# Kernel tuning notes

Measured on AMD Instinct MI355X. Metric: run time of the kernel, lower is better.

## Reference

```python
import jax, jax.numpy as jnp
import numpy as np

N, NFEAT, NHID, NCLASS = 2048, 128, 32, 16

def setup_inputs() -> dict:
    key = jax.random.key(0)
    ks = jax.random.split(key, 12)
    scale = 1.0 / np.sqrt(N)
    inp = {
        "x_init": jax.random.normal(ks[0], (N, NFEAT), jnp.float32),
        "adj": jax.random.uniform(ks[1], (N, N), jnp.float32),
        "adj1_org": jax.random.normal(ks[2], (N, N), jnp.float32) * scale,
        "fully_connected_graph": jnp.ones((N, N), jnp.int32),
        # gc1: GraphConvolution(nfeat, nhid)
        "W1": jax.random.normal(ks[3], (NFEAT, NHID), jnp.float32) / np.sqrt(NFEAT),
        "b1": jnp.zeros((NHID,), jnp.float32),
        # gc2: GraphConvolution(nhid + nfeat, nclass)
        "W2": jax.random.normal(ks[4], (NHID + NFEAT, NCLASS), jnp.float32) / np.sqrt(NHID + NFEAT),
        "b2": jnp.zeros((NCLASS,), jnp.float32),
        # confidence: Linear(2*nhid, nhid) -> Linear(nhid, 1)
        "Wc1": jax.random.normal(ks[5], (2 * NHID, NHID), jnp.float32) / np.sqrt(2 * NHID),
        "bc1": jnp.zeros((NHID,), jnp.float32),
        "Wc2": jax.random.normal(ks[6], (NHID, 1), jnp.float32) / np.sqrt(NHID),
        "bc2": jnp.zeros((1,), jnp.float32),
    }
    return inp

def reference(x_init, adj, adj1_org, fully_connected_graph,
              W1, b1, W2, b2, Wc1, bc1, Wc2, bc2):
    # gc1: adj1_org @ (x_init @ W1) + b1, then tanh (dropout is identity in eval)
    x = jnp.tanh(adj1_org @ (x_init @ W1) + b1)  # [N, nhid]
    # confidence MLP over pairwise concat([x_i, x_j]):
    # Linear(cat([xi,xj])) == xi@Wa + xj@Wb + bc1, with Wc1 = [Wa; Wb]
    Wa, Wb = jnp.split(Wc1, 2, axis=0)
    hidden = (x @ Wa + bc1)[:, None, :] + (x @ Wb)[None, :, :]  # [N, N, nhid]
    e = hidden @ Wc2[:, 0] + bc2[0]  # [N, N] edge score
    # masked_fill(e > 0, 1) then squeeze
    scores = jnp.where(e > 0, 1.0, e)
    adj1 = adj1_org * scores
    xc = jnp.concatenate([x, x_init], axis=-1)  # [N, nhid + nfeat]
    out = adj1 @ (xc @ W2) + b2  # [N, nclass]
    return jax.nn.log_softmax(out, axis=1)
```

## Files before the change

kernel.cpp:

```cpp
#include <hip/hip_runtime.h>
#include <hip/hip_bf16.h>
#include <math.h>

#define N 2048
#define NFEAT 128
#define NHID 32
#define NCLASS 16
#define NSTRIP 16
#define KS 128

#define WS_T1    0
#define WS_Y0    65536
#define WS_WA    98304
#define WS_WB    98336
#define WS_CB    98368
#define WS_PART2 98432
#define WS_Y     1147008
#define WS_PC    1179776
#define WS_Q     1181824
#define WS_PART3 1183872

__global__ __launch_bounds__(256) void k1_prep(
    const float* __restrict__ x_init, const float* __restrict__ W1,
    const float* __restrict__ W2, const float* __restrict__ Wc1,
    const float* __restrict__ bc1, const float* __restrict__ Wc2,
    const float* __restrict__ bc2, float* __restrict__ ws)
{
    __shared__ float xs[8 * 128];
    __shared__ float W1s[128 * 32];
    __shared__ float W2bs[128 * 16];
    int t = threadIdx.x;
    int blk = blockIdx.x;

    *reinterpret_cast<float4*>(&xs[4 * t]) =
        *reinterpret_cast<const float4*>(&x_init[blk * 1024 + 4 * t]);
    #pragma unroll
    for (int i = 0; i < 4; ++i) {
        int f = t + 256 * i;
        *reinterpret_cast<float4*>(&W1s[4 * f]) =
            *reinterpret_cast<const float4*>(&W1[4 * f]);
    }
    #pragma unroll
    for (int i = 0; i < 2; ++i) {
        int f = t + 256 * i;
        *reinterpret_cast<float4*>(&W2bs[4 * f]) =
            *reinterpret_cast<const float4*>(&W2[512 + 4 * f]);
    }
    __syncthreads();

    int rl = t >> 5, c = t & 31;
    int r = blk * 8 + rl;

    float acc = 0.f;
    #pragma unroll 8
    for (int k = 0; k < 128; ++k) acc = fmaf(xs[rl * 128 + k], W1s[k * 32 + c], acc);
    ws[WS_T1 + r * 32 + c] = acc;

    if (c < 16) {
        float a2 = 0.f;
        #pragma unroll 8
        for (int k = 0; k < 128; ++k) a2 = fmaf(xs[rl * 128 + k], W2bs[k * 16 + c], a2);
        ws[WS_Y0 + r * 16 + c] = a2;
    }

    if (blk == 0 && t < 32) {
        float wa = 0.f, wb = 0.f;
        for (int h = 0; h < 32; ++h) {
            float w = Wc2[h];
            wa = fmaf(Wc1[t * 32 + h], w, wa);
            wb = fmaf(Wc1[(32 + t) * 32 + h], w, wb);
        }
        ws[WS_WA + t] = wa;
        ws[WS_WB + t] = wb;
        if (t == 0) {
            float cb = bc2[0];
            for (int h = 0; h < 32; ++h) cb = fmaf(bc1[h], Wc2[h], cb);
            ws[WS_CB] = cb;
        }
    }
}

__global__ __launch_bounds__(256, 2) void k2_mm(
    const float* __restrict__ A, const float* __restrict__ ws_in,
    float* __restrict__ ws_out)
{
    __shared__ float As[64][132];
    __shared__ float Bs[128][32];

    const float* t1 = ws_in + WS_T1;
    int t = threadIdx.x;
    int rt = blockIdx.x >> 4;
    int ks = blockIdx.x & 15;
    int row0 = rt * 64;
    int jbase = ks * KS;

    #pragma unroll
    for (int i = 0; i < 8; ++i) {
        int f = t + 256 * i;
        int r = f >> 5, c4 = f & 31;
        float4 v = *reinterpret_cast<const float4*>(
            &A[(size_t)(row0 + r) * N + jbase + 4 * c4]);
        *reinterpret_cast<float4*>(&As[r][4 * c4]) = v;
    }
    #pragma unroll
    for (int i = 0; i < 4; ++i) {
        int f = t + 256 * i;
        int r = f >> 3, c4 = f & 7;
        float4 v = *reinterpret_cast<const float4*>(&t1[(jbase + r) * 32 + 4 * c4]);
        *reinterpret_cast<float4*>(&Bs[r][4 * c4]) = v;
    }
    __syncthreads();

    int cg = t & 7;
    int rg = t >> 3;

    float acc0[4] = {0.f, 0.f, 0.f, 0.f};
    float acc1[4] = {0.f, 0.f, 0.f, 0.f};

    #pragma unroll
    for (int kq = 0; kq < 32; ++kq) {
        float4 a0 = *reinterpret_cast<const float4*>(&As[rg][4 * kq]);
        float4 a1 = *reinterpret_cast<const float4*>(&As[rg + 32][4 * kq]);
        float4 b0 = *reinterpret_cast<const float4*>(&Bs[4 * kq + 0][4 * cg]);
        float4 b1 = *reinterpret_cast<const float4*>(&Bs[4 * kq + 1][4 * cg]);
        float4 b2 = *reinterpret_cast<const float4*>(&Bs[4 * kq + 2][4 * cg]);
        float4 b3 = *reinterpret_cast<const float4*>(&Bs[4 * kq + 3][4 * cg]);

        acc0[0] = fmaf(a0.x, b0.x, acc0[0]); acc0[1] = fmaf(a0.x, b0.y, acc0[1]);
        acc0[2] = fmaf(a0.x, b0.z, acc0[2]); acc0[3] = fmaf(a0.x, b0.w, acc0[3]);
        acc1[0] = fmaf(a1.x, b0.x, acc1[0]); acc1[1] = fmaf(a1.x, b0.y, acc1[1]);
        acc1[2] = fmaf(a1.x, b0.z, acc1[2]); acc1[3] = fmaf(a1.x, b0.w, acc1[3]);

        acc0[0] = fmaf(a0.y, b1.x, acc0[0]); acc0[1] = fmaf(a0.y, b1.y, acc0[1]);
        acc0[2] = fmaf(a0.y, b1.z, acc0[2]); acc0[3] = fmaf(a0.y, b1.w, acc0[3]);
        acc1[0] = fmaf(a1.y, b1.x, acc1[0]); acc1[1] = fmaf(a1.y, b1.y, acc1[1]);
        acc1[2] = fmaf(a1.y, b1.z, acc1[2]); acc1[3] = fmaf(a1.y, b1.w, acc1[3]);

        acc0[0] = fmaf(a0.z, b2.x, acc0[0]); acc0[1] = fmaf(a0.z, b2.y, acc0[1]);
        acc0[2] = fmaf(a0.z, b2.z, acc0[2]); acc0[3] = fmaf(a0.z, b2.w, acc0[3]);
        acc1[0] = fmaf(a1.z, b2.x, acc1[0]); acc1[1] = fmaf(a1.z, b2.y, acc1[1]);
        acc1[2] = fmaf(a1.z, b2.z, acc1[2]); acc1[3] = fmaf(a1.z, b2.w, acc1[3]);

        acc0[0] = fmaf(a0.w, b3.x, acc0[0]); acc0[1] = fmaf(a0.w, b3.y, acc0[1]);
        acc0[2] = fmaf(a0.w, b3.z, acc0[2]); acc0[3] = fmaf(a0.w, b3.w, acc0[3]);
        acc1[0] = fmaf(a1.w, b3.x, acc1[0]); acc1[1] = fmaf(a1.w, b3.y, acc1[1]);
        acc1[2] = fmaf(a1.w, b3.z, acc1[2]); acc1[3] = fmaf(a1.w, b3.w, acc1[3]);
    }

    float* o0 = ws_out + WS_PART2 + ((size_t)(ks * N + row0 + rg)) * 32 + 4 * cg;
    float* o1 = ws_out + WS_PART2 + ((size_t)(ks * N + row0 + rg + 32)) * 32 + 4 * cg;
    *reinterpret_cast<float4*>(o0) = make_float4(acc0[0], acc0[1], acc0[2], acc0[3]);
    *reinterpret_cast<float4*>(o1) = make_float4(acc1[0], acc1[1], acc1[2], acc1[3]);
}

__global__ __launch_bounds__(256) void k2b_post(
    const float* __restrict__ b1, const float* __restrict__ W2,
    float* __restrict__ ws)
{
    __shared__ float xs[8][32];
    int t = threadIdx.x;
    int rl = t >> 5, c = t & 31;
    int r = blockIdx.x * 8 + rl;

    const float* p2 = ws + WS_PART2;
    float s = b1[c];
    #pragma unroll
    for (int ks = 0; ks < NSTRIP; ++ks)
        s += p2[(size_t)(ks * N + r) * 32 + c];
    float x = tanhf(s);
    xs[rl][c] = x;
    __syncthreads();

    float pp = x * ws[WS_WA + c];
    float qq = x * ws[WS_WB + c];
    #pragma unroll
    for (int d = 1; d < 32; d <<= 1) {
        pp += __shfl_xor(pp, d);
        qq += __shfl_xor(qq, d);
    }
    if (c == 0) {
        ws[WS_PC + r] = pp + ws[WS_CB];
        ws[WS_Q + r] = qq;
    }

    if (c < 16) {
        float acc = ws[WS_Y0 + r * 16 + c];
        #pragma unroll 8
        for (int h = 0; h < 32; ++h) acc = fmaf(xs[rl][h], W2[h * 16 + c], acc);
        ws[WS_Y + r * 16 + c] = acc;
    }
}

__global__ __launch_bounds__(256, 2) void k3_mm(
    const float* __restrict__ A, const float* __restrict__ ws_in,
    float* __restrict__ ws_out)
{
    __shared__ float As[64][132];
    __shared__ float Bs[128][16];

    const float* y = ws_in + WS_Y;
    const float* qv = ws_in + WS_Q;
    const float* pc = ws_in + WS_PC;
    int t = threadIdx.x;
    int rt = blockIdx.x >> 4;
    int ks = blockIdx.x & 15;
    int row0 = rt * 64;
    int jbase = ks * KS;

    #pragma unroll
    for (int i = 0; i < 8; ++i) {
        int f = t + 256 * i;
        int r = f >> 5, c4 = f & 31;
        int j0 = jbase + 4 * c4;
        float4 a = *reinterpret_cast<const float4*>(&A[(size_t)(row0 + r) * N + j0]);
        float4 q4 = *reinterpret_cast<const float4*>(&qv[j0]);
        float pcr = pc[row0 + r];
        float e0 = pcr + q4.x, e1 = pcr + q4.y, e2 = pcr + q4.z, e3 = pcr + q4.w;
        float4 cf;
        cf.x = a.x * ((e0 > 0.f) ? 1.f : e0);
        cf.y = a.y * ((e1 > 0.f) ? 1.f : e1);
        cf.z = a.z * ((e2 > 0.f) ? 1.f : e2);
        cf.w = a.w * ((e3 > 0.f) ? 1.f : e3);
        *reinterpret_cast<float4*>(&As[r][4 * c4]) = cf;
    }
    #pragma unroll
    for (int i = 0; i < 2; ++i) {
        int f = t + 256 * i;
        int r = f >> 2, c4 = f & 3;
        float4 v = *reinterpret_cast<const float4*>(&y[(jbase + r) * 16 + 4 * c4]);
        *reinterpret_cast<float4*>(&Bs[r][4 * c4]) = v;
    }
    __syncthreads();

    int cg = t & 3;
    int rg = t >> 2;

    float acc[4] = {0.f, 0.f, 0.f, 0.f};

    #pragma unroll
    for (int kq = 0; kq < 32; ++kq) {
        float4 a = *reinterpret_cast<const float4*>(&As[rg][4 * kq]);
        float4 b0 = *reinterpret_cast<const float4*>(&Bs[4 * kq + 0][4 * cg]);
        float4 b1 = *reinterpret_cast<const float4*>(&Bs[4 * kq + 1][4 * cg]);
        float4 b2 = *reinterpret_cast<const float4*>(&Bs[4 * kq + 2][4 * cg]);
        float4 b3 = *reinterpret_cast<const float4*>(&Bs[4 * kq + 3][4 * cg]);

        acc[0] = fmaf(a.x, b0.x, acc[0]); acc[1] = fmaf(a.x, b0.y, acc[1]);
        acc[2] = fmaf(a.x, b0.z, acc[2]); acc[3] = fmaf(a.x, b0.w, acc[3]);
        acc[0] = fmaf(a.y, b1.x, acc[0]); acc[1] = fmaf(a.y, b1.y, acc[1]);
        acc[2] = fmaf(a.y, b1.z, acc[2]); acc[3] = fmaf(a.y, b1.w, acc[3]);
        acc[0] = fmaf(a.z, b2.x, acc[0]); acc[1] = fmaf(a.z, b2.y, acc[1]);
        acc[2] = fmaf(a.z, b2.z, acc[2]); acc[3] = fmaf(a.z, b2.w, acc[3]);
        acc[0] = fmaf(a.w, b3.x, acc[0]); acc[1] = fmaf(a.w, b3.y, acc[1]);
        acc[2] = fmaf(a.w, b3.z, acc[2]); acc[3] = fmaf(a.w, b3.w, acc[3]);
    }

    float* o = ws_out + WS_PART3 + ((size_t)(ks * N + row0 + rg)) * 16 + 4 * cg;
    *reinterpret_cast<float4*>(o) = make_float4(acc[0], acc[1], acc[2], acc[3]);
}

__global__ __launch_bounds__(256) void k3b_lsm(
    const float* __restrict__ b2, const float* __restrict__ ws,
    float* __restrict__ out)
{
    int t = threadIdx.x;
    int rl = t >> 4, c = t & 15;
    int r = blockIdx.x * 16 + rl;

    const float* p3 = ws + WS_PART3;
    float o = b2[c];
    #pragma unroll
    for (int ks = 0; ks < NSTRIP; ++ks)
        o += p3[(size_t)(ks * N + r) * 16 + c];

    float m = o;
    #pragma unroll
    for (int d = 1; d < 16; d <<= 1) m = fmaxf(m, __shfl_xor(m, d));
    float ex = expf(o - m);
    float sm = ex;
    #pragma unroll
    for (int d = 1; d < 16; d <<= 1) sm += __shfl_xor(sm, d);

    out[r * 16 + c] = o - m - logf(sm);
}

extern "C" void kernel_launch(void* const* d_in, const int* in_sizes, int n_in,
                              void* d_out, int out_size, void* d_ws, size_t ws_size,
                              hipStream_t stream)
{
    const float* x_init = (const float*)d_in[0];
    const float* adj1   = (const float*)d_in[2];
    const float* W1  = (const float*)d_in[4];
    const float* b1  = (const float*)d_in[5];
    const float* W2  = (const float*)d_in[6];
    const float* b2  = (const float*)d_in[7];
    const float* Wc1 = (const float*)d_in[8];
    const float* bc1 = (const float*)d_in[9];
    const float* Wc2 = (const float*)d_in[10];
    const float* bc2 = (const float*)d_in[11];
    float* out = (float*)d_out;
    float* ws = (float*)d_ws;

    hipLaunchKernelGGL(k1_prep, dim3(256), dim3(256), 0, stream,
                       x_init, W1, W2, Wc1, bc1, Wc2, bc2, ws);
    hipLaunchKernelGGL(k2_mm, dim3(512), dim3(256), 0, stream, adj1, ws, ws);
    hipLaunchKernelGGL(k2b_post, dim3(256), dim3(256), 0, stream, b1, W2, ws);
    hipLaunchKernelGGL(k3_mm, dim3(512), dim3(256), 0, stream, adj1, ws, ws);
    hipLaunchKernelGGL(k3b_lsm, dim3(128), dim3(256), 0, stream, b2, ws, out);
}
```

Measured before the change: 123.0 us.

## Retile split-K matmuls to 128x64 tiles with 32 strips and XOR-swizzled LDS

Both adjacency matmul kernels now use 128-row by 64-column tiles with 32 K-strips instead of 64x128 with 16 strips. Each thread computes more rows, and the A tile in shared memory is stored with an XOR swizzle in place of padding to avoid bank conflicts. The intent is more reuse of B per A load and fewer LDS conflicts. In exchange, the partial-sum buffers double in size and the reduction kernels must sum twice as many strips.

```diff
diff --git a/kernel.cpp b/kernel.cpp
--- a/kernel.cpp
+++ b/kernel.cpp
@@ -6,8 +6,8 @@
 #define NFEAT 128
 #define NHID 32
 #define NCLASS 16
-#define NSTRIP 16
-#define KS 128
+#define NSTRIP 32
+#define KS 64
 
 #define WS_T1    0
 #define WS_Y0    65536
@@ -15,10 +15,10 @@
 #define WS_WB    98336
 #define WS_CB    98368
 #define WS_PART2 98432
-#define WS_Y     1147008
-#define WS_PC    1179776
-#define WS_Q     1181824
-#define WS_PART3 1183872
+#define WS_Y     2195584
+#define WS_PC    2228352
+#define WS_Q     2230400
+#define WS_PART3 2232448
 
 __global__ __launch_bounds__(256) void k1_prep(
     const float* __restrict__ x_init, const float* __restrict__ W1,
@@ -84,73 +84,100 @@
     const float* __restrict__ A, const float* __restrict__ ws_in,
     float* __restrict__ ws_out)
 {
-    __shared__ float As[64][132];
-    __shared__ float Bs[128][32];
+    __shared__ float As[128 * 64];
+    __shared__ float Bs[64 * 32];
 
     const float* t1 = ws_in + WS_T1;
     int t = threadIdx.x;
-    int rt = blockIdx.x >> 4;
-    int ks = blockIdx.x & 15;
-    int row0 = rt * 64;
+    int rt = blockIdx.x >> 5;
+    int ks = blockIdx.x & 31;
+    int row0 = rt * 128;
     int jbase = ks * KS;
 
     #pragma unroll
     for (int i = 0; i < 8; ++i) {
         int f = t + 256 * i;
-        int r = f >> 5, c4 = f & 31;
+        int r = f >> 4, u = f & 15;
         float4 v = *reinterpret_cast<const float4*>(
-            &A[(size_t)(row0 + r) * N + jbase + 4 * c4]);
-        *reinterpret_cast<float4*>(&As[r][4 * c4]) = v;
-    }
-    #pragma unroll
-    for (int i = 0; i < 4; ++i) {
+            &A[(size_t)(row0 + r) * N + jbase + 4 * u]);
+        *reinterpret_cast<float4*>(&As[4 * (r * 16 + (u ^ (r & 7)))]) = v;
+    }
+    #pragma unroll
+    for (int i = 0; i < 2; ++i) {
         int f = t + 256 * i;
         int r = f >> 3, c4 = f & 7;
         float4 v = *reinterpret_cast<const float4*>(&t1[(jbase + r) * 32 + 4 * c4]);
-        *reinterpret_cast<float4*>(&Bs[r][4 * c4]) = v;
+        *reinterpret_cast<float4*>(&Bs[r * 32 + 4 * c4]) = v;
     }
     __syncthreads();
 
+    int rg = t >> 3;
     int cg = t & 7;
-    int rg = t >> 3;
+    int rsw = rg & 7;
 
     float acc0[4] = {0.f, 0.f, 0.f, 0.f};
     float acc1[4] = {0.f, 0.f, 0.f, 0.f};
-
-    #pragma unroll
-    for (int kq = 0; kq < 32; ++kq) {
-        float4 a0 = *reinterpret_cast<const float4*>(&As[rg][4 * kq]);
-        float4 a1 = *reinterpret_cast<const float4*>(&As[rg + 32][4 * kq]);
-        float4 b0 = *reinterpret_cast<const float4*>(&Bs[4 * kq + 0][4 * cg]);
-        float4 b1 = *reinterpret_cast<const float4*>(&Bs[4 * kq + 1][4 * cg]);
-        float4 b2 = *reinterpret_cast<const float4*>(&Bs[4 * kq + 2][4 * cg]);
-        float4 b3 = *reinterpret_cast<const float4*>(&Bs[4 * kq + 3][4 * cg]);
+    float acc2[4] = {0.f, 0.f, 0.f, 0.f};
+    float acc3[4] = {0.f, 0.f, 0.f, 0.f};
+
+    #pragma unroll
+    for (int kq = 0; kq < 16; ++kq) {
+        int ku = kq ^ rsw;
+        float4 a0 = *reinterpret_cast<const float4*>(&As[4 * ((rg +  0) * 16 + ku)]);
+        float4 a1 = *reinterpret_cast<const float4*>(&As[4 * ((rg + 32) * 16 + ku)]);
+        float4 a2 = *reinterpret_cast<const float4*>(&As[4 * ((rg + 64) * 16 + ku)]);
+        float4 a3 = *reinterpret_cast<const float4*>(&As[4 * ((rg + 96) * 16 + ku)]);
+        float4 b0 = *reinterpret_cast<const float4*>(&Bs[(4 * kq + 0) * 32 + 4 * cg]);
+        float4 b1 = *reinterpret_cast<const float4*>(&Bs[(4 * kq + 1) * 32 + 4 * cg]);
+        float4 b2 = *reinterpret_cast<const float4*>(&Bs[(4 * kq + 2) * 32 + 4 * cg]);
+        float4 b3 = *reinterpret_cast<const float4*>(&Bs[(4 * kq + 3) * 32 + 4 * cg]);
 
         acc0[0] = fmaf(a0.x, b0.x, acc0[0]); acc0[1] = fmaf(a0.x, b0.y, acc0[1]);
         acc0[2] = fmaf(a0.x, b0.z, acc0[2]); acc0[3] = fmaf(a0.x, b0.w, acc0[3]);
+        acc0[0] = fmaf(a0.y, b1.x, acc0[0]); acc0[1] = fmaf(a0.y, b1.y, acc0[1]);
+        acc0[2] = fmaf(a0.y, b1.z, acc0[2]); acc0[3] = fmaf(a0.y, b1.w, acc0[3]);
+        acc0[0] = fmaf(a0.z, b2.x, acc0[0]); acc0[1] = fmaf(a0.z, b2.y, acc0[1]);
+        acc0[2] = fmaf(a0.z, b2.z, acc0[2]); acc0[3] = fmaf(a0.z, b2.w, acc0[3]);
+        acc0[0] = fmaf(a0.w, b3.x, acc0[0]); acc0[1] = fmaf(a0.w, b3.y, acc0[1]);
+        acc0[2] = fmaf(a0.w, b3.z, acc0[2]); acc0[3] = fmaf(a0.w, b3.w, acc0[3]);
+
         acc1[0] = fmaf(a1.x, b0.x, acc1[0]); acc1[1] = fmaf(a1.x, b0.y, acc1[1]);
         acc1[2] = fmaf(a1.x, b0.z, acc1[2]); acc1[3] = fmaf(a1.x, b0.w, acc1[3]);
-
-        acc0[0] = fmaf(a0.y, b1.x, acc0[0]); acc0[1] = fmaf(a0.y, b1.y, acc0[1]);
-        acc0[2] = fmaf(a0.y, b1.z, acc0[2]); acc0[3] = fmaf(a0.y, b1.w, acc0[3]);
         acc1[0] = fmaf(a1.y, b1.x, acc1[0]); acc1[1] = fmaf(a1.y, b1.y, acc1[1]);
         acc1[2] = fmaf(a1.y, b1.z, acc1[2]); acc1[3] = fmaf(a1.y, b1.w, acc1[3]);
-
-        acc0[0] = fmaf(a0.z, b2.x, acc0[0]); acc0[1] = fmaf(a0.z, b2.y, acc0[1]);
-        acc0[2] = fmaf(a0.z, b2.z, acc0[2]); acc0[3] = fmaf(a0.z, b2.w, acc0[3]);
         acc1[0] = fmaf(a1.z, b2.x, acc1[0]); acc1[1] = fmaf(a1.z, b2.y, acc1[1]);
         acc1[2] = fmaf(a1.z, b2.z, acc1[2]); acc1[3] = fmaf(a1.z, b2.w, acc1[3]);
-
-        acc0[0] = fmaf(a0.w, b3.x, acc0[0]); acc0[1] = fmaf(a0.w, b3.y, acc0[1]);
-        acc0[2] = fmaf(a0.w, b3.z, acc0[2]); acc0[3] = fmaf(a0.w, b3.w, acc0[3]);
         acc1[0] = fmaf(a1.w, b3.x, acc1[0]); acc1[1] = fmaf(a1.w, b3.y, acc1[1]);
         acc1[2] = fmaf(a1.w, b3.z, acc1[2]); acc1[3] = fmaf(a1.w, b3.w, acc1[3]);
-    }
-
-    float* o0 = ws_out + WS_PART2 + ((size_t)(ks * N + row0 + rg)) * 32 + 4 * cg;
-    float* o1 = ws_out + WS_PART2 + ((size_t)(ks * N + row0 + rg + 32)) * 32 + 4 * cg;
-    *reinterpret_cast<float4*>(o0) = make_float4(acc0[0], acc0[1], acc0[2], acc0[3]);
-    *reinterpret_cast<float4*>(o1) = make_float4(acc1[0], acc1[1], acc1[2], acc1[3]);
+
+        acc2[0] = fmaf(a2.x, b0.x, acc2[0]); acc2[1] = fmaf(a2.x, b0.y, acc2[1]);
+        acc2[2] = fmaf(a2.x, b0.z, acc2[2]); acc2[3] = fmaf(a2.x, b0.w, acc2[3]);
+        acc2[0] = fmaf(a2.y, b1.x, acc2[0]); acc2[1] = fmaf(a2.y, b1.y, acc2[1]);
+        acc2[2] = fmaf(a2.y, b1.z, acc2[2]); acc2[3] = fmaf(a2.y, b1.w, acc2[3]);
+        acc2[0] = fmaf(a2.z, b2.x, acc2[0]); acc2[1] = fmaf(a2.z, b2.y, acc2[1]);
+        acc2[2] = fmaf(a2.z, b2.z, acc2[2]); acc2[3] = fmaf(a2.z, b2.w, acc2[3]);
+        acc2[0] = fmaf(a2.w, b3.x, acc2[0]); acc2[1] = fmaf(a2.w, b3.y, acc2[1]);
+        acc2[2] = fmaf(a2.w, b3.z, acc2[2]); acc2[3] = fmaf(a2.w, b3.w, acc2[3]);
+
+        acc3[0] = fmaf(a3.x, b0.x, acc3[0]); acc3[1] = fmaf(a3.x, b0.y, acc3[1]);
+        acc3[2] = fmaf(a3.x, b0.z, acc3[2]); acc3[3] = fmaf(a3.x, b0.w, acc3[3]);
+        acc3[0] = fmaf(a3.y, b1.x, acc3[0]); acc3[1] = fmaf(a3.y, b1.y, acc3[1]);
+        acc3[2] = fmaf(a3.y, b1.z, acc3[2]); acc3[3] = fmaf(a3.y, b1.w, acc3[3]);
+        acc3[0] = fmaf(a3.z, b2.x, acc3[0]); acc3[1] = fmaf(a3.z, b2.y, acc3[1]);
+        acc3[2] = fmaf(a3.z, b2.z, acc3[2]); acc3[3] = fmaf(a3.z, b2.w, acc3[3]);
+        acc3[0] = fmaf(a3.w, b3.x, acc3[0]); acc3[1] = fmaf(a3.w, b3.y, acc3[1]);
+        acc3[2] = fmaf(a3.w, b3.z, acc3[2]); acc3[3] = fmaf(a3.w, b3.w, acc3[3]);
+    }
+
+    float* base = ws_out + WS_PART2 + ((size_t)ks * N) * 32 + 4 * cg;
+    *reinterpret_cast<float4*>(base + (size_t)(row0 + rg +  0) * 32) =
+        make_float4(acc0[0], acc0[1], acc0[2], acc0[3]);
+    *reinterpret_cast<float4*>(base + (size_t)(row0 + rg + 32) * 32) =
+        make_float4(acc1[0], acc1[1], acc1[2], acc1[3]);
+    *reinterpret_cast<float4*>(base + (size_t)(row0 + rg + 64) * 32) =
+        make_float4(acc2[0], acc2[1], acc2[2], acc2[3]);
+    *reinterpret_cast<float4*>(base + (size_t)(row0 + rg + 96) * 32) =
+        make_float4(acc3[0], acc3[1], acc3[2], acc3[3]);
 }
 
 __global__ __launch_bounds__(256) void k2b_post(
@@ -195,23 +222,23 @@
     const float* __restrict__ A, const float* __restrict__ ws_in,
     float* __restrict__ ws_out)
 {
-    __shared__ float As[64][132];
-    __shared__ float Bs[128][16];
+    __shared__ float As[128 * 64];
+    __shared__ float Bs[64 * 16];
 
     const float* y = ws_in + WS_Y;
     const float* qv = ws_in + WS_Q;
     const float* pc = ws_in + WS_PC;
     int t = threadIdx.x;
-    int rt = blockIdx.x >> 4;
-    int ks = blockIdx.x & 15;
-    int row0 = rt * 64;
+    int rt = blockIdx.x >> 5;
+    int ks = blockIdx.x & 31;
+    int row0 = rt * 128;
     int jbase = ks * KS;
 
     #pragma unroll
     for (int i = 0; i < 8; ++i) {
         int f = t + 256 * i;
-        int r = f >> 5, c4 = f & 31;
-        int j0 = jbase + 4 * c4;
+        int r = f >> 4, u = f & 15;
+        int j0 = jbase + 4 * u;
         float4 a = *reinterpret_cast<const float4*>(&A[(size_t)(row0 + r) * N + j0]);
         float4 q4 = *reinterpret_cast<const float4*>(&qv[j0]);
         float pcr = pc[row0 + r];
@@ -221,42 +248,56 @@
         cf.y = a.y * ((e1 > 0.f) ? 1.f : e1);
         cf.z = a.z * ((e2 > 0.f) ? 1.f : e2);
         cf.w = a.w * ((e3 > 0.f) ? 1.f : e3);
-        *reinterpret_cast<float4*>(&As[r][4 * c4]) = cf;
-    }
-    #pragma unroll
-    for (int i = 0; i < 2; ++i) {
-        int f = t + 256 * i;
-        int r = f >> 2, c4 = f & 3;
+        *reinterpret_cast<float4*>(&As[4 * (r * 16 + (u ^ (r & 7)))]) = cf;
+    }
+    {
+        int r = t >> 2, c4 = t & 3;
         float4 v = *reinterpret_cast<const float4*>(&y[(jbase + r) * 16 + 4 * c4]);
-        *reinterpret_cast<float4*>(&Bs[r][4 * c4]) = v;
+        *reinterpret_cast<float4*>(&Bs[r * 16 + 4 * c4]) = v;
     }
     __syncthreads();
 
+    int rg = t >> 2;
     int cg = t & 3;
-    int rg = t >> 2;
-
-    float acc[4] = {0.f, 0.f, 0.f, 0.f};
-
-    #pragma unroll
-    for (int kq = 0; kq < 32; ++kq) {
-        float4 a = *reinterpret_cast<const float4*>(&As[rg][4 * kq]);
-        float4 b0 = *reinterpret_cast<const float4*>(&Bs[4 * kq + 0][4 * cg]);
-        float4 b1 = *reinterpret_cast<const float4*>(&Bs[4 * kq + 1][4 * cg]);
-        float4 b2 = *reinterpret_cast<const float4*>(&Bs[4 * kq + 2][4 * cg]);
-        float4 b3 = *reinterpret_cast<const float4*>(&Bs[4 * kq + 3][4 * cg]);
-
-        acc[0] = fmaf(a.x, b0.x, acc[0]); acc[1] = fmaf(a.x, b0.y, acc[1]);
-        acc[2] = fmaf(a.x, b0.z, acc[2]); acc[3] = fmaf(a.x, b0.w, acc[3]);
-        acc[0] = fmaf(a.y, b1.x, acc[0]); acc[1] = fmaf(a.y, b1.y, acc[1]);
-        acc[2] = fmaf(a.y, b1.z, acc[2]); acc[3] = fmaf(a.y, b1.w, acc[3]);
-        acc[0] = fmaf(a.z, b2.x, acc[0]); acc[1] = fmaf(a.z, b2.y, acc[1]);
-        acc[2] = fmaf(a.z, b2.z, acc[2]); acc[3] = fmaf(a.z, b2.w, acc[3]);
-        acc[0] = fmaf(a.w, b3.x, acc[0]); acc[1] = fmaf(a.w, b3.y, acc[1]);
-        acc[2] = fmaf(a.w, b3.z, acc[2]); acc[3] = fmaf(a.w, b3.w, acc[3]);
-    }
-
-    float* o = ws_out + WS_PART3 + ((size_t)(ks * N + row0 + rg)) * 16 + 4 * cg;
-    *reinterpret_cast<float4*>(o) = make_float4(acc[0], acc[1], acc[2], acc[3]);
+    int rsw = rg & 7;
+
+    float acc0[4] = {0.f, 0.f, 0.f, 0.f};
+    float acc1[4] = {0.f, 0.f, 0.f, 0.f};
+
+    #pragma unroll
+    for (int kq = 0; kq < 16; ++kq) {
+        int ku = kq ^ rsw;
+        float4 a0 = *reinterpret_cast<const float4*>(&As[4 * ((rg +  0) * 16 + ku)]);
+        float4 a1 = *reinterpret_cast<const float4*>(&As[4 * ((rg + 64) * 16 + ku)]);
+        float4 b0 = *reinterpret_cast<const float4*>(&Bs[(4 * kq + 0) * 16 + 4 * cg]);
+        float4 b1 = *reinterpret_cast<const float4*>(&Bs[(4 * kq + 1) * 16 + 4 * cg]);
+        float4 b2 = *reinterpret_cast<const float4*>(&Bs[(4 * kq + 2) * 16 + 4 * cg]);
+        float4 b3 = *reinterpret_cast<const float4*>(&Bs[(4 * kq + 3) * 16 + 4 * cg]);
+
+        acc0[0] = fmaf(a0.x, b0.x, acc0[0]); acc0[1] = fmaf(a0.x, b0.y, acc0[1]);
+        acc0[2] = fmaf(a0.x, b0.z, acc0[2]); acc0[3] = fmaf(a0.x, b0.w, acc0[3]);
+        acc0[0] = fmaf(a0.y, b1.x, acc0[0]); acc0[1] = fmaf(a0.y, b1.y, acc0[1]);
+        acc0[2] = fmaf(a0.y, b1.z, acc0[2]); acc0[3] = fmaf(a0.y, b1.w, acc0[3]);
+        acc0[0] = fmaf(a0.z, b2.x, acc0[0]); acc0[1] = fmaf(a0.z, b2.y, acc0[1]);
+        acc0[2] = fmaf(a0.z, b2.z, acc0[2]); acc0[3] = fmaf(a0.z, b2.w, acc0[3]);
+        acc0[0] = fmaf(a0.w, b3.x, acc0[0]); acc0[1] = fmaf(a0.w, b3.y, acc0[1]);
+        acc0[2] = fmaf(a0.w, b3.z, acc0[2]); acc0[3] = fmaf(a0.w, b3.w, acc0[3]);
+
+        acc1[0] = fmaf(a1.x, b0.x, acc1[0]); acc1[1] = fmaf(a1.x, b0.y, acc1[1]);
+        acc1[2] = fmaf(a1.x, b0.z, acc1[2]); acc1[3] = fmaf(a1.x, b0.w, acc1[3]);
+        acc1[0] = fmaf(a1.y, b1.x, acc1[0]); acc1[1] = fmaf(a1.y, b1.y, acc1[1]);
+        acc1[2] = fmaf(a1.y, b1.z, acc1[2]); acc1[3] = fmaf(a1.y, b1.w, acc1[3]);
+        acc1[0] = fmaf(a1.z, b2.x, acc1[0]); acc1[1] = fmaf(a1.z, b2.y, acc1[1]);
+        acc1[2] = fmaf(a1.z, b2.z, acc1[2]); acc1[3] = fmaf(a1.z, b2.w, acc1[3]);
+        acc1[0] = fmaf(a1.w, b3.x, acc1[0]); acc1[1] = fmaf(a1.w, b3.y, acc1[1]);
+        acc1[2] = fmaf(a1.w, b3.z, acc1[2]); acc1[3] = fmaf(a1.w, b3.w, acc1[3]);
+    }
+
+    float* base = ws_out + WS_PART3 + ((size_t)ks * N) * 16 + 4 * cg;
+    *reinterpret_cast<float4*>(base + (size_t)(row0 + rg +  0) * 16) =
+        make_float4(acc0[0], acc0[1], acc0[2], acc0[3]);
+    *reinterpret_cast<float4*>(base + (size_t)(row0 + rg + 64) * 16) =
+        make_float4(acc1[0], acc1[1], acc1[2], acc1[3]);
 }
 
 __global__ __launch_bounds__(256) void k3b_lsm(
```

New measurement: 124.0 us. No clear change (+0.8%).

## Fuse split-K reductions into matmul kernels via last-block atomic counters

Applied to the files above, without the earlier changes.

Removes the separate k2b_post and k3b_lsm kernels. The last block to finish each row tile, detected with a per-tile atomic counter and threadfences, now does the partial-sum reduction, tanh, projections and log-softmax for that tile. This cuts two kernel launches and their launch gaps. The cost is a serialized tail, since only 32 blocks do the reduction work, plus atomic and fence overhead. Counters are reset in k1_prep, with 32 threads zeroing 32 entries.

```diff
diff --git a/kernel.cpp b/kernel.cpp
--- a/kernel.cpp
+++ b/kernel.cpp
@@ -19,6 +19,8 @@
 #define WS_PC    1179776
 #define WS_Q     1181824
 #define WS_PART3 1183872
+#define WS_CTR2  1708160
+#define WS_CTR3  1708192
 
 __global__ __launch_bounds__(256) void k1_prep(
     const float* __restrict__ x_init, const float* __restrict__ W1,
@@ -72,6 +74,8 @@
         }
         ws[WS_WA + t] = wa;
         ws[WS_WB + t] = wb;
+        reinterpret_cast<int*>(ws + WS_CTR2)[t] = 0;
+        reinterpret_cast<int*>(ws + WS_CTR3)[t] = 0;
         if (t == 0) {
             float cb = bc2[0];
             for (int h = 0; h < 32; ++h) cb = fmaf(bc1[h], Wc2[h], cb);
@@ -81,13 +85,13 @@
 }
 
 __global__ __launch_bounds__(256, 2) void k2_mm(
-    const float* __restrict__ A, const float* __restrict__ ws_in,
-    float* __restrict__ ws_out)
+    const float* __restrict__ A, const float* __restrict__ b1,
+    const float* __restrict__ W2, float* __restrict__ ws)
 {
     __shared__ float As[64][132];
     __shared__ float Bs[128][32];
 
-    const float* t1 = ws_in + WS_T1;
+    const float* t1 = ws + WS_T1;
     int t = threadIdx.x;
     int rt = blockIdx.x >> 4;
     int ks = blockIdx.x & 15;
@@ -122,85 +126,95 @@
         float4 a0 = *reinterpret_cast<const float4*>(&As[rg][4 * kq]);
         float4 a1 = *reinterpret_cast<const float4*>(&As[rg + 32][4 * kq]);
         float4 b0 = *reinterpret_cast<const float4*>(&Bs[4 * kq + 0][4 * cg]);
-        float4 b1 = *reinterpret_cast<const float4*>(&Bs[4 * kq + 1][4 * cg]);
-        float4 b2 = *reinterpret_cast<const float4*>(&Bs[4 * kq + 2][4 * cg]);
-        float4 b3 = *reinterpret_cast<const float4*>(&Bs[4 * kq + 3][4 * cg]);
+        float4 b1v = *reinterpret_cast<const float4*>(&Bs[4 * kq + 1][4 * cg]);
+        float4 b2v = *reinterpret_cast<const float4*>(&Bs[4 * kq + 2][4 * cg]);
+        float4 b3v = *reinterpret_cast<const float4*>(&Bs[4 * kq + 3][4 * cg]);
 
         acc0[0] = fmaf(a0.x, b0.x, acc0[0]); acc0[1] = fmaf(a0.x, b0.y, acc0[1]);
         acc0[2] = fmaf(a0.x, b0.z, acc0[2]); acc0[3] = fmaf(a0.x, b0.w, acc0[3]);
         acc1[0] = fmaf(a1.x, b0.x, acc1[0]); acc1[1] = fmaf(a1.x, b0.y, acc1[1]);
         acc1[2] = fmaf(a1.x, b0.z, acc1[2]); acc1[3] = fmaf(a1.x, b0.w, acc1[3]);
 
-        acc0[0] = fmaf(a0.y, b1.x, acc0[0]); acc0[1] = fmaf(a0.y, b1.y, acc0[1]);
-        acc0[2] = fmaf(a0.y, b1.z, acc0[2]); acc0[3] = fmaf(a0.y, b1.w, acc0[3]);
-        acc1[0] = fmaf(a1.y, b1.x, acc1[0]); acc1[1] = fmaf(a1.y, b1.y, acc1[1]);
-        acc1[2] = fmaf(a1.y, b1.z, acc1[2]); acc1[3] = fmaf(a1.y, b1.w, acc1[3]);
-
-        acc0[0] = fmaf(a0.z, b2.x, acc0[0]); acc0[1] = fmaf(a0.z, b2.y, acc0[1]);
-        acc0[2] = fmaf(a0.z, b2.z, acc0[2]); acc0[3] = fmaf(a0.z, b2.w, acc0[3]);
-        acc1[0] = fmaf(a1.z, b2.x, acc1[0]); acc1[1] = fmaf(a1.z, b2.y, acc1[1]);
-        acc1[2] = fmaf(a1.z, b2.z, acc1[2]); acc1[3] = fmaf(a1.z, b2.w, acc1[3]);
-
-        acc0[0] = fmaf(a0.w, b3.x, acc0[0]); acc0[1] = fmaf(a0.w, b3.y, acc0[1]);
-        acc0[2] = fmaf(a0.w, b3.z, acc0[2]); acc0[3] = fmaf(a0.w, b3.w, acc0[3]);
-        acc1[0] = fmaf(a1.w, b3.x, acc1[0]); acc1[1] = fmaf(a1.w, b3.y, acc1[1]);
-        acc1[2] = fmaf(a1.w, b3.z, acc1[2]); acc1[3] = fmaf(a1.w, b3.w, acc1[3]);
-    }
-
-    float* o0 = ws_out + WS_PART2 + ((size_t)(ks * N + row0 + rg)) * 32 + 4 * cg;
-    float* o1 = ws_out + WS_PART2 + ((size_t)(ks * N + row0 + rg + 32)) * 32 + 4 * cg;
+        acc0[0] = fmaf(a0.y, b1v.x, acc0[0]); acc0[1] = fmaf(a0.y, b1v.y, acc0[1]);
+        acc0[2] = fmaf(a0.y, b1v.z, acc0[2]); acc0[3] = fmaf(a0.y, b1v.w, acc0[3]);
+        acc1[0] = fmaf(a1.y, b1v.x, acc1[0]); acc1[1] = fmaf(a1.y, b1v.y, acc1[1]);
+        acc1[2] = fmaf(a1.y, b1v.z, acc1[2]); acc1[3] = fmaf(a1.y, b1v.w, acc1[3]);
+
+        acc0[0] = fmaf(a0.z, b2v.x, acc0[0]); acc0[1] = fmaf(a0.z, b2v.y, acc0[1]);
+        acc0[2] = fmaf(a0.z, b2v.z, acc0[2]); acc0[3] = fmaf(a0.z, b2v.w, acc0[3]);
+        acc1[0] = fmaf(a1.z, b2v.x, acc1[0]); acc1[1] = fmaf(a1.z, b2v.y, acc1[1]);
+        acc1[2] = fmaf(a1.z, b2v.z, acc1[2]); acc1[3] = fmaf(a1.z, b2v.w, acc1[3]);
+
+        acc0[0] = fmaf(a0.w, b3v.x, acc0[0]); acc0[1] = fmaf(a0.w, b3v.y, acc0[1]);
+        acc0[2] = fmaf(a0.w, b3v.z, acc0[2]); acc0[3] = fmaf(a0.w, b3v.w, acc0[3]);
+        acc1[0] = fmaf(a1.w, b3v.x, acc1[0]); acc1[1] = fmaf(a1.w, b3v.y, acc1[1]);
+        acc1[2] = fmaf(a1.w, b3v.z, acc1[2]); acc1[3] = fmaf(a1.w, b3v.w, acc1[3]);
+    }
+
+    float* o0 = ws + WS_PART2 + ((size_t)(ks * N + row0 + rg)) * 32 + 4 * cg;
+    float* o1 = ws + WS_PART2 + ((size_t)(ks * N + row0 + rg + 32)) * 32 + 4 * cg;
     *reinterpret_cast<float4*>(o0) = make_float4(acc0[0], acc0[1], acc0[2], acc0[3]);
     *reinterpret_cast<float4*>(o1) = make_float4(acc1[0], acc1[1], acc1[2], acc1[3]);
+
+    __threadfence();
+    __syncthreads();
+    __shared__ int lastFlag;
+    if (t == 0) {
+        int* ctr = reinterpret_cast<int*>(ws + WS_CTR2);
+        lastFlag = (atomicAdd(&ctr[rt], 1) == NSTRIP - 1);
+    }
+    __syncthreads();
+    if (!lastFlag) return;
+    __threadfence();
+
+    __shared__ float xr[8][33];
+    const float* p2 = ws + WS_PART2;
+    int rl = t >> 5, c = t & 31;
+    float wa = ws[WS_WA + c];
+    float wb = ws[WS_WB + c];
+    float cb = ws[WS_CB];
+
+    for (int it = 0; it < 8; ++it) {
+        int r = row0 + it * 8 + rl;
+        float s = b1[c];
+        #pragma unroll
+        for (int k2s = 0; k2s < NSTRIP; ++k2s)
+            s += p2[(size_t)(k2s * N + r) * 32 + c];
+        float x = tanhf(s);
+        xr[rl][c] = x;
+        __syncthreads();
+
+        float pp = x * wa;
+        float qq = x * wb;
+        #pragma unroll
+        for (int d = 1; d < 32; d <<= 1) {
+            pp += __shfl_xor(pp, d);
+            qq += __shfl_xor(qq, d);
+        }
+        if (c == 0) {
+            ws[WS_PC + r] = pp + cb;
+            ws[WS_Q + r] = qq;
+        }
+        if (c < 16) {
+            float acc = ws[WS_Y0 + r * 16 + c];
+            #pragma unroll 8
+            for (int h = 0; h < 32; ++h) acc = fmaf(xr[rl][h], W2[h * 16 + c], acc);
+            ws[WS_Y + r * 16 + c] = acc;
+        }
+        __syncthreads();
+    }
 }
 
-__global__ __launch_bounds__(256) void k2b_post(
-    const float* __restrict__ b1, const float* __restrict__ W2,
-    float* __restrict__ ws)
-{
-    __shared__ float xs[8][32];
-    int t = threadIdx.x;
-    int rl = t >> 5, c = t & 31;
-    int r = blockIdx.x * 8 + rl;
-
-    const float* p2 = ws + WS_PART2;
-    float s = b1[c];
-    #pragma unroll
-    for (int ks = 0; ks < NSTRIP; ++ks)
-        s += p2[(size_t)(ks * N + r) * 32 + c];
-    float x = tanhf(s);
-    xs[rl][c] = x;
-    __syncthreads();
-
-    float pp = x * ws[WS_WA + c];
-    float qq = x * ws[WS_WB + c];
-    #pragma unroll
-    for (int d = 1; d < 32; d <<= 1) {
-        pp += __shfl_xor(pp, d);
-        qq += __shfl_xor(qq, d);
-    }
-    if (c == 0) {
-        ws[WS_PC + r] = pp + ws[WS_CB];
-        ws[WS_Q + r] = qq;
-    }
-
-    if (c < 16) {
-        float acc = ws[WS_Y0 + r * 16 + c];
-        #pragma unroll 8
-        for (int h = 0; h < 32; ++h) acc = fmaf(xs[rl][h], W2[h * 16 + c], acc);
-        ws[WS_Y + r * 16 + c] = acc;
-    }
-}
-
 __global__ __launch_bounds__(256, 2) void k3_mm(
-    const float* __restrict__ A, const float* __restrict__ ws_in,
-    float* __restrict__ ws_out)
+    const float* __restrict__ A, const float* __restrict__ b2,
+    float* __restrict__ ws, float* __restrict__ out)
 {
     __shared__ float As[64][132];
     __shared__ float Bs[128][16];
 
-    const float* y = ws_in + WS_Y;
-    const float* qv = ws_in + WS_Q;
-    const float* pc = ws_in + WS_PC;
+    const float* y = ws + WS_Y;
+    const float* qv = ws + WS_Q;
+    const float* pc = ws + WS_PC;
     int t = threadIdx.x;
     int rt = blockIdx.x >> 4;
     int ks = blockIdx.x & 15;
@@ -241,47 +255,54 @@
     for (int kq = 0; kq < 32; ++kq) {
         float4 a = *reinterpret_cast<const float4*>(&As[rg][4 * kq]);
         float4 b0 = *reinterpret_cast<const float4*>(&Bs[4 * kq + 0][4 * cg]);
-        float4 b1 = *reinterpret_cast<const float4*>(&Bs[4 * kq + 1][4 * cg]);
-        float4 b2 = *reinterpret_cast<const float4*>(&Bs[4 * kq + 2][4 * cg]);
-        float4 b3 = *reinterpret_cast<const float4*>(&Bs[4 * kq + 3][4 * cg]);
+        float4 b1v = *reinterpret_cast<const float4*>(&Bs[4 * kq + 1][4 * cg]);
+        float4 b2v = *reinterpret_cast<const float4*>(&Bs[4 * kq + 2][4 * cg]);
+        float4 b3v = *reinterpret_cast<const float4*>(&Bs[4 * kq + 3][4 * cg]);
 
         acc[0] = fmaf(a.x, b0.x, acc[0]); acc[1] = fmaf(a.x, b0.y, acc[1]);
         acc[2] = fmaf(a.x, b0.z, acc[2]); acc[3] = fmaf(a.x, b0.w, acc[3]);
-        acc[0] = fmaf(a.y, b1.x, acc[0]); acc[1] = fmaf(a.y, b1.y, acc[1]);
-        acc[2] = fmaf(a.y, b1.z, acc[2]); acc[3] = fmaf(a.y, b1.w, acc[3]);
-        acc[0] = fmaf(a.z, b2.x, acc[0]); acc[1] = fmaf(a.z, b2.y, acc[1]);
-        acc[2] = fmaf(a.z, b2.z, acc[2]); acc[3] = fmaf(a.z, b2.w, acc[3]);
-        acc[0] = fmaf(a.w, b3.x, acc[0]); acc[1] = fmaf(a.w, b3.y, acc[1]);
-        acc[2] = fmaf(a.w, b3.z, acc[2]); acc[3] = fmaf(a.w, b3.w, acc[3]);
-    }
-
-    float* o = ws_out + WS_PART3 + ((size_t)(ks * N + row0 + rg)) * 16 + 4 * cg;
+        acc[0] = fmaf(a.y, b1v.x, acc[0]); acc[1] = fmaf(a.y, b1v.y, acc[1]);
+        acc[2] = fmaf(a.y, b1v.z, acc[2]); acc[3] = fmaf(a.y, b1v.w, acc[3]);
+        acc[0] = fmaf(a.z, b2v.x, acc[0]); acc[1] = fmaf(a.z, b2v.y, acc[1]);
+        acc[2] = fmaf(a.z, b2v.z, acc[2]); acc[3] = fmaf(a.z, b2v.w, acc[3]);
+        acc[0] = fmaf(a.w, b3v.x, acc[0]); acc[1] = fmaf(a.w, b3v.y, acc[1]);
+        acc[2] = fmaf(a.w, b3v.z, acc[2]); acc[3] = fmaf(a.w, b3v.w, acc[3]);
+    }
+
+    float* o = ws + WS_PART3 + ((size_t)(ks * N + row0 + rg)) * 16 + 4 * cg;
     *reinterpret_cast<float4*>(o) = make_float4(acc[0], acc[1], acc[2], acc[3]);
-}
-
-__global__ __launch_bounds__(256) void k3b_lsm(
-    const float* __restrict__ b2, const float* __restrict__ ws,
-    float* __restrict__ out)
-{
-    int t = threadIdx.x;
+
+    __threadfence();
+    __syncthreads();
+    __shared__ int lastFlag;
+    if (t == 0) {
+        int* ctr = reinterpret_cast<int*>(ws + WS_CTR3);
+        lastFlag = (atomicAdd(&ctr[rt], 1) == NSTRIP - 1);
+    }
+    __syncthreads();
+    if (!lastFlag) return;
+    __threadfence();
+
+    const float* p3 = ws + WS_PART3;
     int rl = t >> 4, c = t & 15;
-    int r = blockIdx.x * 16 + rl;
-
-    const float* p3 = ws + WS_PART3;
-    float o = b2[c];
-    #pragma unroll
-    for (int ks = 0; ks < NSTRIP; ++ks)
-        o += p3[(size_t)(ks * N + r) * 16 + c];
-
-    float m = o;
-    #pragma unroll
-    for (int d = 1; d < 16; d <<= 1) m = fmaxf(m, __shfl_xor(m, d));
-    float ex = expf(o - m);
-    float sm = ex;
-    #pragma unroll
-    for (int d = 1; d < 16; d <<= 1) sm += __shfl_xor(sm, d);
-
-    out[r * 16 + c] = o - m - logf(sm);
+
+    for (int it = 0; it < 4; ++it) {
+        int r = row0 + it * 16 + rl;
+        float o2 = b2[c];
+        #pragma unroll
+        for (int k3s = 0; k3s < NSTRIP; ++k3s)
+            o2 += p3[(size_t)(k3s * N + r) * 16 + c];
+
+        float m = o2;
+        #pragma unroll
+        for (int d = 1; d < 16; d <<= 1) m = fmaxf(m, __shfl_xor(m, d));
+        float ex = expf(o2 - m);
+        float sm = ex;
+        #pragma unroll
+        for (int d = 1; d < 16; d <<= 1) sm += __shfl_xor(sm, d);
+
+        out[r * 16 + c] = o2 - m - logf(sm);
+    }
 }
 
 extern "C" void kernel_launch(void* const* d_in, const int* in_sizes, int n_in,
@@ -303,8 +324,6 @@
 
     hipLaunchKernelGGL(k1_prep, dim3(256), dim3(256), 0, stream,
                        x_init, W1, W2, Wc1, bc1, Wc2, bc2, ws);
-    hipLaunchKernelGGL(k2_mm, dim3(512), dim3(256), 0, stream, adj1, ws, ws);
-    hipLaunchKernelGGL(k2b_post, dim3(256), dim3(256), 0, stream, b1, W2, ws);
-    hipLaunchKernelGGL(k3_mm, dim3(512), dim3(256), 0, stream, adj1, ws, ws);
-    hipLaunchKernelGGL(k3b_lsm, dim3(128), dim3(256), 0, stream, b2, ws, out);
+    hipLaunchKernelGGL(k2_mm, dim3(512), dim3(256), 0, stream, adj1, b1, W2, ws);
+    hipLaunchKernelGGL(k3_mm, dim3(512), dim3(256), 0, stream, adj1, b2, ws, out);
 }
```

Result: slower. 239.9 us (+95.0%).
